# Kernel tuning notes

Hardware: AMD Instinct MI355X
Metric: run time of the kernel (lower is better)

Reference implementation:

```python
import jax, jax.numpy as jnp
import numpy as np

# dims
N = 200000   # n_nodes
D = 256      # node_dim
S = 8        # n_substructures
M = 100000   # gathered atom indices per substructure (flattened detections)
H = 64       # dim_per_substructure
B = 4096     # batch_size (max(batch_idx)+1)


def setup_inputs() -> dict:
    key = jax.random.key(0)
    ks = jax.random.split(key, 8)
    node_features = jax.random.normal(ks[0], (N, D), dtype=jnp.float32)
    sub_indices = jax.random.randint(ks[1], (S, M), 0, N, dtype=jnp.int32)
    batch_idx = jax.random.randint(ks[2], (N,), 0, B, dtype=jnp.int32)
    # per-substructure MLP params: Linear(D,H) -> ReLU -> Linear(H,H)
    s1 = 1.0 / np.sqrt(D)
    s2 = 1.0 / np.sqrt(H)
    W1 = jax.random.uniform(ks[3], (S, D, H), minval=-s1, maxval=s1, dtype=jnp.float32)
    b1 = jax.random.uniform(ks[4], (S, H), minval=-s1, maxval=s1, dtype=jnp.float32)
    W2 = jax.random.uniform(ks[5], (S, H, H), minval=-s2, maxval=s2, dtype=jnp.float32)
    b2 = jax.random.uniform(ks[6], (S, H), minval=-s2, maxval=s2, dtype=jnp.float32)
    return {"node_features": node_features, "W1": W1, "b1": b1, "W2": W2,
            "b2": b2, "sub_indices": sub_indices, "batch_idx": batch_idx}


def reference(node_features, W1, b1, W2, b2, sub_indices, batch_idx):
    # gather node feats per substructure: [S, M, D]
    gathered = node_features[sub_indices]
    # 2-layer MLP per substructure (sum aggregation path of the module)
    h = jax.nn.relu(jnp.einsum('smd,sdh->smh', gathered, W1) + b1[:, None, :])
    enc = jnp.einsum('smh,shk->smk', h, W2) + b2[:, None, :]   # [S, M, H]
    # scatter-add into per-graph slots (index_add_ over batch idx of gathered atoms)
    seg = batch_idx[sub_indices]                               # [S, M]
    agg = jax.vmap(lambda e, s: jax.ops.segment_sum(e, s, num_segments=B))(enc, seg)  # [S, B, H]
    # concatenate per-substructure blocks -> [B, S*H]
    return jnp.transpose(agg, (1, 0, 2)).reshape(B, S * H)
```

## Files before the change

### kernel.cpp

```cpp
#include <hip/hip_runtime.h>

#define Nn 200000
#define Dn 256
#define Hn 64
#define Sn 8
#define Mn 100000
#define Bn 4096

#define RPB 256
#define KC 32
#define NT 256
#define XS 40
#define WS 40

typedef __attribute__((ext_vector_type(8))) short bf16x8;
typedef __attribute__((ext_vector_type(4))) float f32x4;
typedef __attribute__((ext_vector_type(8))) unsigned short u16x8;
typedef __attribute__((ext_vector_type(4))) unsigned short u16x4;

static __device__ __forceinline__ unsigned short f2bf(float x) {
    unsigned u = __float_as_uint(x);
    return (unsigned short)((u + 0x7fffu + ((u >> 16) & 1u)) >> 16);
}
static __device__ __forceinline__ float bf2f(unsigned short h) {
    return __uint_as_float(((unsigned)h) << 16);
}

__global__ __launch_bounds__(NT)
void l1_kernel(const float* __restrict__ nf, const float* __restrict__ W1,
               const float* __restrict__ b1, const int* __restrict__ sub_idx,
               const int* __restrict__ bidx, float* __restrict__ hsum,
               float* __restrict__ cnt)
{
    __shared__ unsigned short Xhi[RPB * XS];
    __shared__ unsigned short Xlo[RPB * XS];
    __shared__ unsigned short Whi[Hn * WS];
    __shared__ unsigned short Wlo[Hn * WS];
    __shared__ int sseg[RPB];

    const int s    = blockIdx.y;
    const int m0   = blockIdx.x * RPB;
    const int tid  = threadIdx.x;
    const int lane = tid & 63;
    const int w    = tid >> 6;
    const int qq   = lane >> 4;
    const int r16  = lane & 15;

    const int  m    = m0 + tid;
    const bool val  = (m < Mn);
    const int  node = val ? sub_idx[(size_t)s * Mn + m] : 0;
    sseg[tid] = val ? bidx[node] : 0;

    const float* xrow = nf + (size_t)node * Dn;

    const int wc = tid & 63;
    const int wq = tid >> 6;

    f32x4 acc[4][4];
#pragma unroll
    for (int mi = 0; mi < 4; ++mi)
#pragma unroll
        for (int ni = 0; ni < 4; ++ni) acc[mi][ni] = (f32x4){0.f, 0.f, 0.f, 0.f};

    for (int kk = 0; kk < Dn; kk += KC) {
        __syncthreads();

        {
            unsigned short hi[KC], lo[KC];
#pragma unroll
            for (int q4 = 0; q4 < KC / 4; ++q4) {
                float4 v = val ? *(const float4*)(xrow + kk + 4 * q4)
                               : make_float4(0.f, 0.f, 0.f, 0.f);
                float xs[4] = {v.x, v.y, v.z, v.w};
#pragma unroll
                for (int e = 0; e < 4; ++e) {
                    unsigned short h = f2bf(xs[e]);
                    hi[4 * q4 + e] = h;
                    lo[4 * q4 + e] = f2bf(xs[e] - bf2f(h));
                }
            }
#pragma unroll
            for (int v8 = 0; v8 < KC / 8; ++v8) {
                *(u16x8*)&Xhi[tid * XS + 8 * v8] = *(const u16x8*)&hi[8 * v8];
                *(u16x8*)&Xlo[tid * XS + 8 * v8] = *(const u16x8*)&lo[8 * v8];
            }
        }
#pragma unroll
        for (int h2 = 0; h2 < 2; ++h2) {
            const int kq = wq + 4 * h2;
            unsigned short whi[4], wlo[4];
#pragma unroll
            for (int i = 0; i < 4; ++i) {
                float wv = W1[((size_t)(s * Dn + kk + 4 * kq + i)) * Hn + wc];
                unsigned short h = f2bf(wv);
                whi[i] = h;
                wlo[i] = f2bf(wv - bf2f(h));
            }
            *(u16x4*)&Whi[wc * WS + 4 * kq] = *(const u16x4*)&whi[0];
            *(u16x4*)&Wlo[wc * WS + 4 * kq] = *(const u16x4*)&wlo[0];
        }
        __syncthreads();

        bf16x8 ah[4], al[4];
#pragma unroll
        for (int mi = 0; mi < 4; ++mi) {
            const int rb = (64 * w + 16 * mi + r16) * XS + 8 * qq;
            ah[mi] = *(const bf16x8*)&Xhi[rb];
            al[mi] = *(const bf16x8*)&Xlo[rb];
        }
#pragma unroll
        for (int ni = 0; ni < 4; ++ni) {
            const int cb = (16 * ni + r16) * WS + 8 * qq;
            bf16x8 bh = *(const bf16x8*)&Whi[cb];
            bf16x8 bl = *(const bf16x8*)&Wlo[cb];
#pragma unroll
            for (int mi = 0; mi < 4; ++mi) {
                acc[mi][ni] = __builtin_amdgcn_mfma_f32_16x16x32_bf16(ah[mi], bh, acc[mi][ni], 0, 0, 0);
                acc[mi][ni] = __builtin_amdgcn_mfma_f32_16x16x32_bf16(ah[mi], bl, acc[mi][ni], 0, 0, 0);
                acc[mi][ni] = __builtin_amdgcn_mfma_f32_16x16x32_bf16(al[mi], bh, acc[mi][ni], 0, 0, 0);
            }
        }
    }

    float bcol[4];
#pragma unroll
    for (int ni = 0; ni < 4; ++ni) bcol[ni] = b1[s * Hn + 16 * ni + r16];

#pragma unroll
    for (int mi = 0; mi < 4; ++mi) {
#pragma unroll
        for (int r = 0; r < 4; ++r) {
            const int row = 64 * w + 16 * mi + 4 * qq + r;
            const int mg  = m0 + row;
            if (mg >= Mn) continue;
            const int sg = sseg[row];
            float* dst = hsum + ((size_t)(s * Bn + sg)) * Hn;
#pragma unroll
            for (int ni = 0; ni < 4; ++ni) {
                float v = fmaxf(acc[mi][ni][r] + bcol[ni], 0.f);
                atomicAdd(dst + 16 * ni + r16, v);
            }
        }
    }
    if (val) atomicAdd(cnt + s * Bn + sseg[tid], 1.0f);
}

__global__ __launch_bounds__(256)
void l2_kernel(const float* __restrict__ hsum, const float* __restrict__ cnt,
               const float* __restrict__ W2, const float* __restrict__ b2,
               float* __restrict__ out)
{
    const int wid  = (int)((blockIdx.x * blockDim.x + threadIdx.x) >> 6);
    const int lane = threadIdx.x & 63;
    if (wid >= Sn * Bn) return;
    const int s = wid >> 12;
    const int b = wid & (Bn - 1);

    float hv = hsum[(size_t)wid * Hn + lane];
    const float* w2 = W2 + (size_t)s * Hn * Hn + lane;

    float acc = 0.f;
#pragma unroll 8
    for (int jj = 0; jj < Hn; ++jj) {
        float x = __shfl(hv, jj);
        acc = fmaf(x, w2[(size_t)jj * Hn], acc);
    }
    float c = cnt[wid];
    float v = acc + c * b2[s * Hn + lane];
    out[(size_t)b * (Sn * Hn) + s * Hn + lane] = v;
}

extern "C" void kernel_launch(void* const* d_in, const int* in_sizes, int n_in,
                              void* d_out, int out_size, void* d_ws, size_t ws_size,
                              hipStream_t stream)
{
    const float* nf   = (const float*)d_in[0];
    const float* W1   = (const float*)d_in[1];
    const float* b1   = (const float*)d_in[2];
    const float* W2   = (const float*)d_in[3];
    const float* b2   = (const float*)d_in[4];
    const int*   sidx = (const int*)d_in[5];
    const int*   bidx = (const int*)d_in[6];
    float* out = (float*)d_out;

    float* hsum = (float*)d_ws;
    float* cnt  = hsum + (size_t)Sn * Bn * Hn;

    hipMemsetAsync(d_ws, 0, ((size_t)Sn * Bn * Hn + (size_t)Sn * Bn) * sizeof(float),
                   stream);

    dim3 g1((Mn + RPB - 1) / RPB, Sn);
    l1_kernel<<<g1, NT, 0, stream>>>(nf, W1, b1, sidx, bidx, hsum, cnt);

    const int rows    = Sn * Bn;
    const int blocks2 = (rows * 64 + 255) / 256;
    l2_kernel<<<blocks2, 256, 0, stream>>>(hsum, cnt, W2, b2, out);
}
```

Measured before the change: 574.1 us.

## Prefetch next K-chunk into registers, cheapen bf16 split, restructure layer-2 kernel

The layer-1 kernel now prefetches the next K-chunk of gathered node features and W1 into registers while the current chunk's MFMAs run. It replaces round-to-nearest bf16 conversion with truncation-based hi/lo splitting that packs two values per word. It also adds a launch-bounds occupancy hint, shrinks the segment cache to 16-bit, and regroups the MFMA issue order. The layer-2 kernel stages W2 in shared memory and lets each wave process four rows, reusing weight loads. Risks are higher register pressure from the prefetch buffers and slightly different rounding in the hi/lo split, which drops the padding-row zeroing for invalid rows (it loads node 0 instead).

```diff
diff --git a/kernel.cpp b/kernel.cpp
--- a/kernel.cpp
+++ b/kernel.cpp
@@ -15,28 +15,28 @@
 
 typedef __attribute__((ext_vector_type(8))) short bf16x8;
 typedef __attribute__((ext_vector_type(4))) float f32x4;
-typedef __attribute__((ext_vector_type(8))) unsigned short u16x8;
-typedef __attribute__((ext_vector_type(4))) unsigned short u16x4;
-
-static __device__ __forceinline__ unsigned short f2bf(float x) {
-    unsigned u = __float_as_uint(x);
-    return (unsigned short)((u + 0x7fffu + ((u >> 16) & 1u)) >> 16);
-}
-static __device__ __forceinline__ float bf2f(unsigned short h) {
-    return __uint_as_float(((unsigned)h) << 16);
-}
-
-__global__ __launch_bounds__(NT)
+
+static __device__ __forceinline__ void split2(float a, float b,
+                                              unsigned& h, unsigned& l) {
+    unsigned ua = __float_as_uint(a), ub = __float_as_uint(b);
+    unsigned ha = ua & 0xFFFF0000u, hb = ub & 0xFFFF0000u;
+    float la = a - __uint_as_float(ha);
+    float lb = b - __uint_as_float(hb);
+    h = (ua >> 16) | hb;
+    l = (__float_as_uint(la) >> 16) | (__float_as_uint(lb) & 0xFFFF0000u);
+}
+
+__global__ __launch_bounds__(NT, 3)
 void l1_kernel(const float* __restrict__ nf, const float* __restrict__ W1,
                const float* __restrict__ b1, const int* __restrict__ sub_idx,
                const int* __restrict__ bidx, float* __restrict__ hsum,
                float* __restrict__ cnt)
 {
-    __shared__ unsigned short Xhi[RPB * XS];
-    __shared__ unsigned short Xlo[RPB * XS];
-    __shared__ unsigned short Whi[Hn * WS];
-    __shared__ unsigned short Wlo[Hn * WS];
-    __shared__ int sseg[RPB];
+    __shared__ __align__(16) unsigned short Xhi[RPB * XS];
+    __shared__ __align__(16) unsigned short Xlo[RPB * XS];
+    __shared__ __align__(16) unsigned short Whi[Hn * WS];
+    __shared__ __align__(16) unsigned short Wlo[Hn * WS];
+    __shared__ unsigned short sseg[RPB];
 
     const int s    = blockIdx.y;
     const int m0   = blockIdx.x * RPB;
@@ -49,7 +49,7 @@
     const int  m    = m0 + tid;
     const bool val  = (m < Mn);
     const int  node = val ? sub_idx[(size_t)s * Mn + m] : 0;
-    sseg[tid] = val ? bidx[node] : 0;
+    sseg[tid] = (unsigned short)(val ? bidx[node] : 0);
 
     const float* xrow = nf + (size_t)node * Dn;
 
@@ -62,44 +62,48 @@
 #pragma unroll
         for (int ni = 0; ni < 4; ++ni) acc[mi][ni] = (f32x4){0.f, 0.f, 0.f, 0.f};
 
-    for (int kk = 0; kk < Dn; kk += KC) {
+    float fx[8 * 4];
+    float fw[8];
+
+    {
+        const float4* xp = (const float4*)xrow;
+#pragma unroll
+        for (int v = 0; v < 8; ++v) *(float4*)&fx[4 * v] = xp[v];
+        const float* wp = W1 + ((size_t)(s * Dn + 8 * wq)) * Hn + wc;
+#pragma unroll
+        for (int i = 0; i < 8; ++i) fw[i] = wp[(size_t)i * Hn];
+    }
+
+    for (int c = 0; c < Dn / KC; ++c) {
         __syncthreads();
 
+#pragma unroll
+        for (int v = 0; v < 4; ++v) {
+            unsigned h[4], l[4];
+#pragma unroll
+            for (int j = 0; j < 4; ++j)
+                split2(fx[8 * v + 2 * j], fx[8 * v + 2 * j + 1], h[j], l[j]);
+            *(uint4*)&Xhi[tid * XS + 8 * v] = make_uint4(h[0], h[1], h[2], h[3]);
+            *(uint4*)&Xlo[tid * XS + 8 * v] = make_uint4(l[0], l[1], l[2], l[3]);
+        }
         {
-            unsigned short hi[KC], lo[KC];
-#pragma unroll
-            for (int q4 = 0; q4 < KC / 4; ++q4) {
-                float4 v = val ? *(const float4*)(xrow + kk + 4 * q4)
-                               : make_float4(0.f, 0.f, 0.f, 0.f);
-                float xs[4] = {v.x, v.y, v.z, v.w};
-#pragma unroll
-                for (int e = 0; e < 4; ++e) {
-                    unsigned short h = f2bf(xs[e]);
-                    hi[4 * q4 + e] = h;
-                    lo[4 * q4 + e] = f2bf(xs[e] - bf2f(h));
-                }
-            }
-#pragma unroll
-            for (int v8 = 0; v8 < KC / 8; ++v8) {
-                *(u16x8*)&Xhi[tid * XS + 8 * v8] = *(const u16x8*)&hi[8 * v8];
-                *(u16x8*)&Xlo[tid * XS + 8 * v8] = *(const u16x8*)&lo[8 * v8];
-            }
-        }
-#pragma unroll
-        for (int h2 = 0; h2 < 2; ++h2) {
-            const int kq = wq + 4 * h2;
-            unsigned short whi[4], wlo[4];
-#pragma unroll
-            for (int i = 0; i < 4; ++i) {
-                float wv = W1[((size_t)(s * Dn + kk + 4 * kq + i)) * Hn + wc];
-                unsigned short h = f2bf(wv);
-                whi[i] = h;
-                wlo[i] = f2bf(wv - bf2f(h));
-            }
-            *(u16x4*)&Whi[wc * WS + 4 * kq] = *(const u16x4*)&whi[0];
-            *(u16x4*)&Wlo[wc * WS + 4 * kq] = *(const u16x4*)&wlo[0];
+            unsigned h[4], l[4];
+#pragma unroll
+            for (int j = 0; j < 4; ++j) split2(fw[2 * j], fw[2 * j + 1], h[j], l[j]);
+            *(uint4*)&Whi[wc * WS + 8 * wq] = make_uint4(h[0], h[1], h[2], h[3]);
+            *(uint4*)&Wlo[wc * WS + 8 * wq] = make_uint4(l[0], l[1], l[2], l[3]);
         }
         __syncthreads();
+
+        if (c + 1 < Dn / KC) {
+            const int kk = (c + 1) * KC;
+            const float4* xp = (const float4*)(xrow + kk);
+#pragma unroll
+            for (int v = 0; v < 8; ++v) *(float4*)&fx[4 * v] = xp[v];
+            const float* wp = W1 + ((size_t)(s * Dn + kk + 8 * wq)) * Hn + wc;
+#pragma unroll
+            for (int i = 0; i < 8; ++i) fw[i] = wp[(size_t)i * Hn];
+        }
 
         bf16x8 ah[4], al[4];
 #pragma unroll
@@ -114,11 +118,14 @@
             bf16x8 bh = *(const bf16x8*)&Whi[cb];
             bf16x8 bl = *(const bf16x8*)&Wlo[cb];
 #pragma unroll
-            for (int mi = 0; mi < 4; ++mi) {
+            for (int mi = 0; mi < 4; ++mi)
                 acc[mi][ni] = __builtin_amdgcn_mfma_f32_16x16x32_bf16(ah[mi], bh, acc[mi][ni], 0, 0, 0);
+#pragma unroll
+            for (int mi = 0; mi < 4; ++mi)
                 acc[mi][ni] = __builtin_amdgcn_mfma_f32_16x16x32_bf16(ah[mi], bl, acc[mi][ni], 0, 0, 0);
+#pragma unroll
+            for (int mi = 0; mi < 4; ++mi)
                 acc[mi][ni] = __builtin_amdgcn_mfma_f32_16x16x32_bf16(al[mi], bh, acc[mi][ni], 0, 0, 0);
-            }
         }
     }
 
@@ -150,24 +157,43 @@
                const float* __restrict__ W2, const float* __restrict__ b2,
                float* __restrict__ out)
 {
-    const int wid  = (int)((blockIdx.x * blockDim.x + threadIdx.x) >> 6);
-    const int lane = threadIdx.x & 63;
-    if (wid >= Sn * Bn) return;
-    const int s = wid >> 12;
-    const int b = wid & (Bn - 1);
-
-    float hv = hsum[(size_t)wid * Hn + lane];
-    const float* w2 = W2 + (size_t)s * Hn * Hn + lane;
-
-    float acc = 0.f;
+    __shared__ float W2s[Hn * Hn];
+    const int s    = blockIdx.y;
+    const int b0   = blockIdx.x * 64;
+    const int tid  = threadIdx.x;
+    const int lane = tid & 63;
+    const int w    = tid >> 6;
+
+    const float* w2g = W2 + (size_t)s * Hn * Hn;
+#pragma unroll
+    for (int i = 0; i < 4; ++i)
+        ((float4*)W2s)[tid + 256 * i] = ((const float4*)w2g)[tid + 256 * i];
+    __syncthreads();
+
+    const float b2v = b2[s * Hn + lane];
+
+#pragma unroll
+    for (int g = 0; g < 4; ++g) {
+        const int rb = b0 + w * 16 + g * 4;
+        float hv[4], ct[4], acc[4];
+#pragma unroll
+        for (int i = 0; i < 4; ++i) {
+            const size_t rr = (size_t)s * Bn + rb + i;
+            hv[i]  = hsum[rr * Hn + lane];
+            ct[i]  = cnt[rr];
+            acc[i] = 0.f;
+        }
 #pragma unroll 8
-    for (int jj = 0; jj < Hn; ++jj) {
-        float x = __shfl(hv, jj);
-        acc = fmaf(x, w2[(size_t)jj * Hn], acc);
-    }
-    float c = cnt[wid];
-    float v = acc + c * b2[s * Hn + lane];
-    out[(size_t)b * (Sn * Hn) + s * Hn + lane] = v;
+        for (int j = 0; j < Hn; ++j) {
+            float wv = W2s[j * Hn + lane];
+#pragma unroll
+            for (int i = 0; i < 4; ++i)
+                acc[i] = fmaf(__shfl(hv[i], j), wv, acc[i]);
+        }
+#pragma unroll
+        for (int i = 0; i < 4; ++i)
+            out[(size_t)(rb + i) * (Sn * Hn) + s * Hn + lane] = acc[i] + ct[i] * b2v;
+    }
 }
 
 extern "C" void kernel_launch(void* const* d_in, const int* in_sizes, int n_in,
@@ -192,7 +218,6 @@
     dim3 g1((Mn + RPB - 1) / RPB, Sn);
     l1_kernel<<<g1, NT, 0, stream>>>(nf, W1, b1, sidx, bidx, hsum, cnt);
 
-    const int rows    = Sn * Bn;
-    const int blocks2 = (rows * 64 + 255) / 256;
-    l2_kernel<<<blocks2, 256, 0, stream>>>(hsum, cnt, W2, b2, out);
-}
+    dim3 g2(Bn / 64, Sn);
+    l2_kernel<<<g2, 256, 0, stream>>>(hsum, cnt, W2, b2, out);
+}
```

Result: faster. 536.2 us (-6.6%).
